# Kernel optimization log

Measured on AMD Instinct MI355X. Metric: run time of the kernel, lower is better.

Reference implementation:

```python
import jax, jax.numpy as jnp
import numpy as np

N = 8192
E = 262144
D_IN = 256
D_OUT = 256

def setup_inputs() -> dict:
    key = jax.random.key(0)
    k1, k2, k3, k4 = jax.random.split(key, 4)
    x = jax.random.normal(k1, (N, D_IN), dtype=jnp.float32)
    edge_index = jax.random.randint(k2, (2, E), 0, N, dtype=jnp.int64)
    W = jax.random.normal(k3, (D_OUT, D_IN), dtype=jnp.float32) * (1.0 / np.sqrt(D_IN))
    b = jax.random.normal(k4, (D_OUT,), dtype=jnp.float32) * 0.01
    return {"x": x, "edge_index": edge_index, "W": W, "b": b}

def reference(x, edge_index, W, b):
    num_nodes = x.shape[0]
    # dense adjacency: adj[src, dst] = 1.0 (duplicates collapse to 1, matching torch assignment)
    adj = jnp.zeros((num_nodes, num_nodes), dtype=x.dtype)
    adj = adj.at[edge_index[0], edge_index[1]].set(1.0)
    adj = adj + jnp.eye(num_nodes, dtype=x.dtype)  # self-loops (may yield 2.0 if edge had self-loop, as in torch)
    deg = adj.sum(axis=1, keepdims=True)           # [N, 1]
    adj_norm = adj / deg                           # row-normalized
    aggregated = adj_norm @ x                      # [N, D_IN]
    return aggregated @ W.T + b                    # linear: [N, D_OUT]
```

## Files before the change

### kernel.cpp

```cpp
#include <hip/hip_runtime.h>
#include <hip/hip_fp16.h>


#define NNODES 8192
#define DFEAT  256
#define WPR    256
#define LISTCAP 2048

typedef __attribute__((ext_vector_type(8))) _Float16 f16x8;
typedef __attribute__((ext_vector_type(4))) _Float16 f16x4;
typedef __attribute__((ext_vector_type(4))) float    f32x4;

__global__ __launch_bounds__(256) void gcn_scatter_wconv(
    const int* __restrict__ ei, int E, unsigned* __restrict__ bitmap,
    const float* __restrict__ W, _Float16* __restrict__ Wh,
    _Float16* __restrict__ Wl) {
  const int nbs = (E + 255) >> 8;
  const int b = blockIdx.x;
  if (b < nbs) {
    int e = b * 256 + threadIdx.x;
    if (e < E) {
      int s = ei[e];
      int d = ei[E + e];
      atomicOr(&bitmap[(size_t)s * WPR + (d >> 5)], 1u << (d & 31));
    }
  } else {
    int i = (b - nbs) * 256 + threadIdx.x;
    if (i < DFEAT * DFEAT / 4) {
      float4 v = *(const float4*)(W + (size_t)i * 4);
      f16x4 h = {(_Float16)v.x, (_Float16)v.y, (_Float16)v.z, (_Float16)v.w};
      f16x4 l = {(_Float16)(v.x - (float)h[0]), (_Float16)(v.y - (float)h[1]),
                 (_Float16)(v.z - (float)h[2]), (_Float16)(v.w - (float)h[3])};
      *(f16x4*)(Wh + (size_t)i * 4) = h;
      *(f16x4*)(Wl + (size_t)i * 4) = l;
    }
  }
}

__global__ __launch_bounds__(256) void gcn_gemm(
    const float* __restrict__ X, const _Float16* __restrict__ Wh,
    const _Float16* __restrict__ Wl, _Float16* __restrict__ Y) {
  const int wave = threadIdx.x >> 6;
  const int lane = threadIdx.x & 63;
  const int row0 = blockIdx.x * 64 + wave * 16;
  const int col0 = blockIdx.y * 64;
  const int lr = lane & 15;
  const int kh = (lane >> 4) * 8;

  f32x4 acc[4];
#pragma unroll
  for (int i = 0; i < 4; ++i) acc[i] = (f32x4){0.f, 0.f, 0.f, 0.f};

  const float*    ap  = X  + (size_t)(row0 + lr) * DFEAT + kh;
  const _Float16* bhp = Wh + (size_t)(col0 + lr) * DFEAT + kh;
  const _Float16* blp = Wl + (size_t)(col0 + lr) * DFEAT + kh;

#pragma unroll
  for (int k0 = 0; k0 < DFEAT; k0 += 32) {
    float4 x0 = *(const float4*)(ap + k0);
    float4 x1 = *(const float4*)(ap + k0 + 4);
    f16x8 a = {(_Float16)x0.x, (_Float16)x0.y, (_Float16)x0.z, (_Float16)x0.w,
               (_Float16)x1.x, (_Float16)x1.y, (_Float16)x1.z, (_Float16)x1.w};
#pragma unroll
    for (int nt = 0; nt < 4; ++nt) {
      f16x8 bh = *(const f16x8*)(bhp + k0 + nt * 16 * DFEAT);
      f16x8 bl = *(const f16x8*)(blp + k0 + nt * 16 * DFEAT);
      acc[nt] = __builtin_amdgcn_mfma_f32_16x16x32_f16(a, bh, acc[nt], 0, 0, 0);
      acc[nt] = __builtin_amdgcn_mfma_f32_16x16x32_f16(a, bl, acc[nt], 0, 0, 0);
    }
  }

  const int crow = row0 + (lane >> 4) * 4;
  const int ccol = col0 + lr;
#pragma unroll
  for (int nt = 0; nt < 4; ++nt)
#pragma unroll
    for (int r = 0; r < 4; ++r)
      Y[(size_t)(crow + r) * DFEAT + ccol + nt * 16] = (_Float16)acc[nt][r];
}

__global__ __launch_bounds__(256) void gcn_aggregate(
    const unsigned* __restrict__ bitmap, const _Float16* __restrict__ Y,
    const float* __restrict__ bias, float* __restrict__ out) {
  __shared__ unsigned short list[LISTCAP];
  __shared__ int cnt;
  const int node = blockIdx.x;
  const int tid  = threadIdx.x;
  if (tid == 0) cnt = 0;
  __syncthreads();

  unsigned w = bitmap[(size_t)node * WPR + tid];
  while (w) {
    int bit = __ffs(w) - 1;
    w &= w - 1;
    int pos = atomicAdd(&cnt, 1);
    if (pos < LISTCAP) list[pos] = (unsigned short)(tid * 32 + bit);
  }
  __syncthreads();

  const int n = min(cnt, LISTCAP);
  float a0 = (float)Y[(size_t)node * DFEAT + tid];
  float a1 = 0.f, a2 = 0.f, a3 = 0.f;
  int k = 0;
  for (; k + 4 <= n; k += 4) {
    int j0 = list[k], j1 = list[k + 1], j2 = list[k + 2], j3 = list[k + 3];
    a0 += (float)Y[(size_t)j0 * DFEAT + tid];
    a1 += (float)Y[(size_t)j1 * DFEAT + tid];
    a2 += (float)Y[(size_t)j2 * DFEAT + tid];
    a3 += (float)Y[(size_t)j3 * DFEAT + tid];
  }
  for (; k < n; ++k) a0 += (float)Y[(size_t)list[k] * DFEAT + tid];

  out[(size_t)node * DFEAT + tid] =
      (a0 + a1 + a2 + a3) / (float)(n + 1) + bias[tid];
}

extern "C" void kernel_launch(void* const* d_in, const int* in_sizes, int n_in,
                              void* d_out, int out_size, void* d_ws, size_t ws_size,
                              hipStream_t stream) {
  const float* x  = (const float*)d_in[0];
  const int*   ei = (const int*)d_in[1];
  const float* W  = (const float*)d_in[2];
  const float* b  = (const float*)d_in[3];
  float* out = (float*)d_out;
  const int E = in_sizes[1] / 2;

  char* p = (char*)d_ws;
  size_t off = 0;
  auto take = [&](size_t bytes) { char* r = p + off; off = (off + bytes + 255) & ~(size_t)255; return r; };
  unsigned* bitmap = (unsigned*) take((size_t)NNODES * WPR * 4);
  _Float16* Wh     = (_Float16*) take((size_t)DFEAT * DFEAT * 2);
  _Float16* Wl     = (_Float16*) take((size_t)DFEAT * DFEAT * 2);
  _Float16* Y      = (_Float16*) take((size_t)NNODES * DFEAT * 2);

  hipMemsetAsync(bitmap, 0, (size_t)NNODES * WPR * 4, stream);

  const int nbs = (E + 255) / 256;
  const int nbw = (DFEAT * DFEAT / 4 + 255) / 256;
  gcn_scatter_wconv<<<nbs + nbw, 256, 0, stream>>>(ei, E, bitmap, W, Wh, Wl);

  gcn_gemm<<<dim3(NNODES / 64, DFEAT / 64), 256, 0, stream>>>(x, Wh, Wl, Y);

  gcn_aggregate<<<NNODES, 256, 0, stream>>>(bitmap, Y, b, out);
}
```

Baseline: 121.6 us.

## Fuse GCN stages into persistent kernel with capped adjacency lists

Replaces the three launches plus bitmap memset with one persistent kernel of 512 blocks. Stages are separated by atomic-counter grid barriers. The dense 8192x8192-bit adjacency bitmap becomes per-node fixed-capacity neighbour lists built with atomic degree counters, and duplicate edges are removed at aggregation time by an in-wave quadratic scan. This drops the large bitmap memset and scan plus the launch gaps. The cost is spin-wait barriers and a degree cap of 192 that silently truncates higher-degree nodes. The control-word reset using a magic value may also race across repeated calls.

```diff
diff --git a/kernel.cpp b/kernel.cpp
--- a/kernel.cpp
+++ b/kernel.cpp
@@ -4,115 +4,164 @@
 
 #define NNODES 8192
 #define DFEAT  256
-#define WPR    256
-#define LISTCAP 2048
+#define MAXDEG 192
+#define NBLK   512
+#define NTHR   256
+#define MAGIC  0x13572468u
 
 typedef __attribute__((ext_vector_type(8))) _Float16 f16x8;
 typedef __attribute__((ext_vector_type(4))) _Float16 f16x4;
 typedef __attribute__((ext_vector_type(4))) float    f32x4;
 
-__global__ __launch_bounds__(256) void gcn_scatter_wconv(
-    const int* __restrict__ ei, int E, unsigned* __restrict__ bitmap,
-    const float* __restrict__ W, _Float16* __restrict__ Wh,
-    _Float16* __restrict__ Wl) {
-  const int nbs = (E + 255) >> 8;
-  const int b = blockIdx.x;
-  if (b < nbs) {
-    int e = b * 256 + threadIdx.x;
-    if (e < E) {
-      int s = ei[e];
-      int d = ei[E + e];
-      atomicOr(&bitmap[(size_t)s * WPR + (d >> 5)], 1u << (d & 31));
+__device__ inline void grid_barrier(unsigned* ctr) {
+  __syncthreads();
+  if (threadIdx.x == 0) {
+    __threadfence();
+    atomicAdd(ctr, 1u);
+    while (atomicAdd(ctr, 0u) < NBLK) __builtin_amdgcn_s_sleep(8);
+    __threadfence();
+  }
+  __syncthreads();
+}
+
+__global__ __launch_bounds__(NTHR, 2) void gcn_all(
+    const float* __restrict__ X, const int* __restrict__ ei,
+    const float* __restrict__ W, const float* __restrict__ bias, int E,
+    unsigned* __restrict__ ctl, int* __restrict__ deg,
+    unsigned short* __restrict__ adj, _Float16* __restrict__ Wh,
+    _Float16* __restrict__ Wl, _Float16* __restrict__ Y,
+    float* __restrict__ out)
+{
+  const int bid  = blockIdx.x, tid = threadIdx.x;
+  const int gtid = bid * NTHR + tid;
+  const int wave = tid >> 6, lane = tid & 63;
+
+  if (gtid < NNODES) deg[gtid] = 0;
+  if (gtid < DFEAT * DFEAT / 4) {
+    float4 v = *(const float4*)(W + (size_t)gtid * 4);
+    f16x4 h = {(_Float16)v.x, (_Float16)v.y, (_Float16)v.z, (_Float16)v.w};
+    f16x4 l = {(_Float16)(v.x - (float)h[0]), (_Float16)(v.y - (float)h[1]),
+               (_Float16)(v.z - (float)h[2]), (_Float16)(v.w - (float)h[3])};
+    *(f16x4*)(Wh + (size_t)gtid * 4) = h;
+    *(f16x4*)(Wl + (size_t)gtid * 4) = l;
+  }
+  if (bid == 0) {
+    __syncthreads();
+    if (tid >= 1 && tid <= 3) ctl[tid * 32] = 0;
+    __syncthreads();
+    if (tid == 0) { __threadfence(); atomicExch(&ctl[0], MAGIC); }
+  }
+  if (tid == 0)
+    while (atomicAdd(&ctl[0], 0u) != MAGIC) __builtin_amdgcn_s_sleep(8);
+  __syncthreads();
+  grid_barrier(&ctl[32]);
+
+  for (int e = gtid; e < E; e += NBLK * NTHR) {
+    int s = ei[e];
+    int d = ei[E + e];
+    int pos = atomicAdd(&deg[s], 1);
+    if (pos < MAXDEG) adj[(size_t)s * MAXDEG + pos] = (unsigned short)d;
+  }
+  grid_barrier(&ctl[64]);
+
+  {
+    const int row0 = (bid >> 2) * 64 + wave * 16;
+    const int col0 = (bid & 3) * 64;
+    const int lr = lane & 15;
+    const int kh = (lane >> 4) * 8;
+
+    f32x4 acc[4];
+#pragma unroll
+    for (int i = 0; i < 4; ++i) acc[i] = (f32x4){0.f, 0.f, 0.f, 0.f};
+
+    const float*    ap  = X  + (size_t)(row0 + lr) * DFEAT + kh;
+    const _Float16* bhp = Wh + (size_t)(col0 + lr) * DFEAT + kh;
+    const _Float16* blp = Wl + (size_t)(col0 + lr) * DFEAT + kh;
+
+#pragma unroll
+    for (int k0 = 0; k0 < DFEAT; k0 += 32) {
+      float4 x0 = *(const float4*)(ap + k0);
+      float4 x1 = *(const float4*)(ap + k0 + 4);
+      f16x8 a = {(_Float16)x0.x, (_Float16)x0.y, (_Float16)x0.z, (_Float16)x0.w,
+                 (_Float16)x1.x, (_Float16)x1.y, (_Float16)x1.z, (_Float16)x1.w};
+#pragma unroll
+      for (int nt = 0; nt < 4; ++nt) {
+        f16x8 bh = *(const f16x8*)(bhp + k0 + nt * 16 * DFEAT);
+        f16x8 bl = *(const f16x8*)(blp + k0 + nt * 16 * DFEAT);
+        acc[nt] = __builtin_amdgcn_mfma_f32_16x16x32_f16(a, bh, acc[nt], 0, 0, 0);
+        acc[nt] = __builtin_amdgcn_mfma_f32_16x16x32_f16(a, bl, acc[nt], 0, 0, 0);
+      }
     }
-  } else {
-    int i = (b - nbs) * 256 + threadIdx.x;
-    if (i < DFEAT * DFEAT / 4) {
-      float4 v = *(const float4*)(W + (size_t)i * 4);
-      f16x4 h = {(_Float16)v.x, (_Float16)v.y, (_Float16)v.z, (_Float16)v.w};
-      f16x4 l = {(_Float16)(v.x - (float)h[0]), (_Float16)(v.y - (float)h[1]),
-                 (_Float16)(v.z - (float)h[2]), (_Float16)(v.w - (float)h[3])};
-      *(f16x4*)(Wh + (size_t)i * 4) = h;
-      *(f16x4*)(Wl + (size_t)i * 4) = l;
+    const int crow = row0 + (lane >> 4) * 4;
+    const int ccol = col0 + lr;
+#pragma unroll
+    for (int nt = 0; nt < 4; ++nt)
+#pragma unroll
+      for (int r = 0; r < 4; ++r)
+        Y[(size_t)(crow + r) * DFEAT + ccol + nt * 16] = (_Float16)acc[nt][r];
+  }
+  grid_barrier(&ctl[96]);
+
+  {
+    __shared__ unsigned short listS[4][MAXDEG];
+    __shared__ unsigned char  keepS[4][MAXDEG];
+    unsigned short* list = listS[wave];
+    unsigned char*  keep = keepS[wave];
+    const int ch4 = lane * 4;
+    const float4 b4 = *(const float4*)(bias + ch4);
+
+    for (int node = bid * 4 + wave; node < NNODES; node += NBLK * 4) {
+      int d = atomicAdd(&deg[node], 0);
+      if (d > MAXDEG) d = MAXDEG;
+
+      for (int base = 0; base < d; base += 64)
+        if (base + lane < d)
+          list[base + lane] = adj[(size_t)node * MAXDEG + base + lane];
+
+      int ndist = 0;
+#pragma unroll
+      for (int base = 0; base < MAXDEG; base += 64) {
+        int idx = base + lane;
+        bool kp = false;
+        if (idx < d) {
+          unsigned short v = list[idx];
+          kp = true;
+          for (int k = 0; k < idx; ++k)
+            if (list[k] == v) { kp = false; break; }
+        }
+        keep[idx] = kp ? 1 : 0;
+        ndist += __popcll(__ballot(kp));
+      }
+
+      f16x4 sv = *(const f16x4*)(Y + (size_t)node * DFEAT + ch4);
+      float ax = (float)sv[0], ay = (float)sv[1], az = (float)sv[2], aw = (float)sv[3];
+
+      int k = 0;
+      for (; k + 4 <= d; k += 4) {
+        int j0 = list[k], j1 = list[k + 1], j2 = list[k + 2], j3 = list[k + 3];
+        float w0 = keep[k], w1 = keep[k + 1], w2 = keep[k + 2], w3 = keep[k + 3];
+        f16x4 r0 = *(const f16x4*)(Y + (size_t)j0 * DFEAT + ch4);
+        f16x4 r1 = *(const f16x4*)(Y + (size_t)j1 * DFEAT + ch4);
+        f16x4 r2 = *(const f16x4*)(Y + (size_t)j2 * DFEAT + ch4);
+        f16x4 r3 = *(const f16x4*)(Y + (size_t)j3 * DFEAT + ch4);
+        ax += w0 * (float)r0[0] + w1 * (float)r1[0] + w2 * (float)r2[0] + w3 * (float)r3[0];
+        ay += w0 * (float)r0[1] + w1 * (float)r1[1] + w2 * (float)r2[1] + w3 * (float)r3[1];
+        az += w0 * (float)r0[2] + w1 * (float)r1[2] + w2 * (float)r2[2] + w3 * (float)r3[2];
+        aw += w0 * (float)r0[3] + w1 * (float)r1[3] + w2 * (float)r2[3] + w3 * (float)r3[3];
+      }
+      for (; k < d; ++k) {
+        float w0 = keep[k];
+        f16x4 r0 = *(const f16x4*)(Y + (size_t)list[k] * DFEAT + ch4);
+        ax += w0 * (float)r0[0]; ay += w0 * (float)r0[1];
+        az += w0 * (float)r0[2]; aw += w0 * (float)r0[3];
+      }
+
+      float inv = 1.f / (float)(ndist + 1);
+      float4 o = {ax * inv + b4.x, ay * inv + b4.y,
+                  az * inv + b4.z, aw * inv + b4.w};
+      *(float4*)(out + (size_t)node * DFEAT + ch4) = o;
     }
   }
-}
-
-__global__ __launch_bounds__(256) void gcn_gemm(
-    const float* __restrict__ X, const _Float16* __restrict__ Wh,
-    const _Float16* __restrict__ Wl, _Float16* __restrict__ Y) {
-  const int wave = threadIdx.x >> 6;
-  const int lane = threadIdx.x & 63;
-  const int row0 = blockIdx.x * 64 + wave * 16;
-  const int col0 = blockIdx.y * 64;
-  const int lr = lane & 15;
-  const int kh = (lane >> 4) * 8;
-
-  f32x4 acc[4];
-#pragma unroll
-  for (int i = 0; i < 4; ++i) acc[i] = (f32x4){0.f, 0.f, 0.f, 0.f};
-
-  const float*    ap  = X  + (size_t)(row0 + lr) * DFEAT + kh;
-  const _Float16* bhp = Wh + (size_t)(col0 + lr) * DFEAT + kh;
-  const _Float16* blp = Wl + (size_t)(col0 + lr) * DFEAT + kh;
-
-#pragma unroll
-  for (int k0 = 0; k0 < DFEAT; k0 += 32) {
-    float4 x0 = *(const float4*)(ap + k0);
-    float4 x1 = *(const float4*)(ap + k0 + 4);
-    f16x8 a = {(_Float16)x0.x, (_Float16)x0.y, (_Float16)x0.z, (_Float16)x0.w,
-               (_Float16)x1.x, (_Float16)x1.y, (_Float16)x1.z, (_Float16)x1.w};
-#pragma unroll
-    for (int nt = 0; nt < 4; ++nt) {
-      f16x8 bh = *(const f16x8*)(bhp + k0 + nt * 16 * DFEAT);
-      f16x8 bl = *(const f16x8*)(blp + k0 + nt * 16 * DFEAT);
-      acc[nt] = __builtin_amdgcn_mfma_f32_16x16x32_f16(a, bh, acc[nt], 0, 0, 0);
-      acc[nt] = __builtin_amdgcn_mfma_f32_16x16x32_f16(a, bl, acc[nt], 0, 0, 0);
-    }
-  }
-
-  const int crow = row0 + (lane >> 4) * 4;
-  const int ccol = col0 + lr;
-#pragma unroll
-  for (int nt = 0; nt < 4; ++nt)
-#pragma unroll
-    for (int r = 0; r < 4; ++r)
-      Y[(size_t)(crow + r) * DFEAT + ccol + nt * 16] = (_Float16)acc[nt][r];
-}
-
-__global__ __launch_bounds__(256) void gcn_aggregate(
-    const unsigned* __restrict__ bitmap, const _Float16* __restrict__ Y,
-    const float* __restrict__ bias, float* __restrict__ out) {
-  __shared__ unsigned short list[LISTCAP];
-  __shared__ int cnt;
-  const int node = blockIdx.x;
-  const int tid  = threadIdx.x;
-  if (tid == 0) cnt = 0;
-  __syncthreads();
-
-  unsigned w = bitmap[(size_t)node * WPR + tid];
-  while (w) {
-    int bit = __ffs(w) - 1;
-    w &= w - 1;
-    int pos = atomicAdd(&cnt, 1);
-    if (pos < LISTCAP) list[pos] = (unsigned short)(tid * 32 + bit);
-  }
-  __syncthreads();
-
-  const int n = min(cnt, LISTCAP);
-  float a0 = (float)Y[(size_t)node * DFEAT + tid];
-  float a1 = 0.f, a2 = 0.f, a3 = 0.f;
-  int k = 0;
-  for (; k + 4 <= n; k += 4) {
-    int j0 = list[k], j1 = list[k + 1], j2 = list[k + 2], j3 = list[k + 3];
-    a0 += (float)Y[(size_t)j0 * DFEAT + tid];
-    a1 += (float)Y[(size_t)j1 * DFEAT + tid];
-    a2 += (float)Y[(size_t)j2 * DFEAT + tid];
-    a3 += (float)Y[(size_t)j3 * DFEAT + tid];
-  }
-  for (; k < n; ++k) a0 += (float)Y[(size_t)list[k] * DFEAT + tid];
-
-  out[(size_t)node * DFEAT + tid] =
-      (a0 + a1 + a2 + a3) / (float)(n + 1) + bias[tid];
 }
 
 extern "C" void kernel_launch(void* const* d_in, const int* in_sizes, int n_in,
@@ -128,18 +177,12 @@
   char* p = (char*)d_ws;
   size_t off = 0;
   auto take = [&](size_t bytes) { char* r = p + off; off = (off + bytes + 255) & ~(size_t)255; return r; };
-  unsigned* bitmap = (unsigned*) take((size_t)NNODES * WPR * 4);
-  _Float16* Wh     = (_Float16*) take((size_t)DFEAT * DFEAT * 2);
-  _Float16* Wl     = (_Float16*) take((size_t)DFEAT * DFEAT * 2);
-  _Float16* Y      = (_Float16*) take((size_t)NNODES * DFEAT * 2);
+  unsigned*       ctl = (unsigned*)       take(512);
+  int*            deg = (int*)            take((size_t)NNODES * 4);
+  unsigned short* adj = (unsigned short*) take((size_t)NNODES * MAXDEG * 2);
+  _Float16*       Wh  = (_Float16*)       take((size_t)DFEAT * DFEAT * 2);
+  _Float16*       Wl  = (_Float16*)       take((size_t)DFEAT * DFEAT * 2);
+  _Float16*       Y   = (_Float16*)       take((size_t)NNODES * DFEAT * 2);
 
-  hipMemsetAsync(bitmap, 0, (size_t)NNODES * WPR * 4, stream);
-
-  const int nbs = (E + 255) / 256;
-  const int nbw = (DFEAT * DFEAT / 4 + 255) / 256;
-  gcn_scatter_wconv<<<nbs + nbw, 256, 0, stream>>>(ei, E, bitmap, W, Wh, Wl);
-
-  gcn_gemm<<<dim3(NNODES / 64, DFEAT / 64), 256, 0, stream>>>(x, Wh, Wl, Y);
-
-  gcn_aggregate<<<NNODES, 256, 0, stream>>>(bitmap, Y, b, out);
+  gcn_all<<<NBLK, NTHR, 0, stream>>>(x, ei, W, b, E, ctl, deg, adj, Wh, Wl, Y, out);
 }
```

New measurement: 262.8 us. 2.16x slower.

## Fuse bitmap zeroing and W conversion into GEMM, wave-per-node aggregation

Applied to the files above, without the earlier changes.

Drops the memset and folds bitmap zeroing into the GEMM kernel. The W fp16 hi/lo split now happens inline in the GEMM, which uses wider 64x128 tiles. Edge scatter becomes its own launch. Aggregation now assigns one wave per node with f16x4 vectorized gathers, and the per-node neighbor list cap drops to 256. This is meant to cut launch count and improve gather efficiency, at the cost of recomputing the W conversion per block and risking truncation for nodes with more than 256 neighbors.

```diff
diff --git a/kernel.cpp b/kernel.cpp
--- a/kernel.cpp
+++ b/kernel.cpp
@@ -5,55 +5,36 @@
 #define NNODES 8192
 #define DFEAT  256
 #define WPR    256
-#define LISTCAP 2048
+#define LISTCAP 256
 
 typedef __attribute__((ext_vector_type(8))) _Float16 f16x8;
 typedef __attribute__((ext_vector_type(4))) _Float16 f16x4;
 typedef __attribute__((ext_vector_type(4))) float    f32x4;
 
-__global__ __launch_bounds__(256) void gcn_scatter_wconv(
-    const int* __restrict__ ei, int E, unsigned* __restrict__ bitmap,
-    const float* __restrict__ W, _Float16* __restrict__ Wh,
-    _Float16* __restrict__ Wl) {
-  const int nbs = (E + 255) >> 8;
-  const int b = blockIdx.x;
-  if (b < nbs) {
-    int e = b * 256 + threadIdx.x;
-    if (e < E) {
-      int s = ei[e];
-      int d = ei[E + e];
-      atomicOr(&bitmap[(size_t)s * WPR + (d >> 5)], 1u << (d & 31));
-    }
-  } else {
-    int i = (b - nbs) * 256 + threadIdx.x;
-    if (i < DFEAT * DFEAT / 4) {
-      float4 v = *(const float4*)(W + (size_t)i * 4);
-      f16x4 h = {(_Float16)v.x, (_Float16)v.y, (_Float16)v.z, (_Float16)v.w};
-      f16x4 l = {(_Float16)(v.x - (float)h[0]), (_Float16)(v.y - (float)h[1]),
-                 (_Float16)(v.z - (float)h[2]), (_Float16)(v.w - (float)h[3])};
-      *(f16x4*)(Wh + (size_t)i * 4) = h;
-      *(f16x4*)(Wl + (size_t)i * 4) = l;
-    }
+__global__ __launch_bounds__(256) void gcn_gemm(
+    const float* __restrict__ X, const float* __restrict__ W,
+    _Float16* __restrict__ Y, uint4* __restrict__ bitmap4) {
+  const int bid = blockIdx.x, tid = threadIdx.x;
+  const int gtid = bid * 256 + tid;
+
+  {
+    const uint4 z = {0u, 0u, 0u, 0u};
+#pragma unroll
+    for (int i = 0; i < 8; ++i) bitmap4[(size_t)gtid * 8 + i] = z;
   }
-}
 
-__global__ __launch_bounds__(256) void gcn_gemm(
-    const float* __restrict__ X, const _Float16* __restrict__ Wh,
-    const _Float16* __restrict__ Wl, _Float16* __restrict__ Y) {
-  const int wave = threadIdx.x >> 6;
-  const int lane = threadIdx.x & 63;
-  const int row0 = blockIdx.x * 64 + wave * 16;
-  const int col0 = blockIdx.y * 64;
+  const int wave = tid >> 6, lane = tid & 63;
+  const int row0 = (bid >> 1) * 64 + wave * 16;
+  const int col0 = (bid & 1) * 128;
   const int lr = lane & 15;
   const int kh = (lane >> 4) * 8;
 
-  f32x4 acc[4];
+  f32x4 acc[8];
 #pragma unroll
-  for (int i = 0; i < 4; ++i) acc[i] = (f32x4){0.f, 0.f, 0.f, 0.f};
+  for (int i = 0; i < 8; ++i) acc[i] = (f32x4){0.f, 0.f, 0.f, 0.f};
 
-  const float*    ap  = X  + (size_t)(row0 + lr) * DFEAT + kh;
-  const _Float16* bhp = Wh + (size_t)(col0 + lr) * DFEAT + kh;
-  const _Float16* blp = Wl + (size_t)(col0 + lr) * DFEAT + kh;
+  const float* ap = X + (size_t)(row0 + lr) * DFEAT + kh;
+  const float* wp = W + (size_t)(col0 + lr) * DFEAT + kh;
 
 #pragma unroll
   for (int k0 = 0; k0 < DFEAT; k0 += 32) {
@@ -62,9 +43,15 @@
     f16x8 a = {(_Float16)x0.x, (_Float16)x0.y, (_Float16)x0.z, (_Float16)x0.w,
                (_Float16)x1.x, (_Float16)x1.y, (_Float16)x1.z, (_Float16)x1.w};
 #pragma unroll
-    for (int nt = 0; nt < 4; ++nt) {
-      f16x8 bh = *(const f16x8*)(bhp + k0 + nt * 16 * DFEAT);
-      f16x8 bl = *(const f16x8*)(blp + k0 + nt * 16 * DFEAT);
+    for (int nt = 0; nt < 8; ++nt) {
+      float4 w0 = *(const float4*)(wp + k0 + nt * 16 * DFEAT);
+      float4 w1 = *(const float4*)(wp + k0 + nt * 16 * DFEAT + 4);
+      f16x8 bh = {(_Float16)w0.x, (_Float16)w0.y, (_Float16)w0.z, (_Float16)w0.w,
+                  (_Float16)w1.x, (_Float16)w1.y, (_Float16)w1.z, (_Float16)w1.w};
+      f16x8 bl = {(_Float16)(w0.x - (float)bh[0]), (_Float16)(w0.y - (float)bh[1]),
+                  (_Float16)(w0.z - (float)bh[2]), (_Float16)(w0.w - (float)bh[3]),
+                  (_Float16)(w1.x - (float)bh[4]), (_Float16)(w1.y - (float)bh[5]),
+                  (_Float16)(w1.z - (float)bh[6]), (_Float16)(w1.w - (float)bh[7])};
       acc[nt] = __builtin_amdgcn_mfma_f32_16x16x32_f16(a, bh, acc[nt], 0, 0, 0);
       acc[nt] = __builtin_amdgcn_mfma_f32_16x16x32_f16(a, bl, acc[nt], 0, 0, 0);
     }
@@ -73,46 +60,83 @@
   const int crow = row0 + (lane >> 4) * 4;
   const int ccol = col0 + lr;
 #pragma unroll
-  for (int nt = 0; nt < 4; ++nt)
+  for (int nt = 0; nt < 8; ++nt)
 #pragma unroll
     for (int r = 0; r < 4; ++r)
       Y[(size_t)(crow + r) * DFEAT + ccol + nt * 16] = (_Float16)acc[nt][r];
 }
 
+__global__ __launch_bounds__(256) void gcn_scatter(
+    const int* __restrict__ ei, int E, unsigned* __restrict__ bitmap) {
+  int e = blockIdx.x * 256 + threadIdx.x;
+  if (e < E) {
+    int s = ei[e];
+    int d = ei[E + e];
+    atomicOr(&bitmap[(size_t)s * WPR + (d >> 5)], 1u << (d & 31));
+  }
+}
+
 __global__ __launch_bounds__(256) void gcn_aggregate(
     const unsigned* __restrict__ bitmap, const _Float16* __restrict__ Y,
     const float* __restrict__ bias, float* __restrict__ out) {
-  __shared__ unsigned short list[LISTCAP];
-  __shared__ int cnt;
-  const int node = blockIdx.x;
-  const int tid  = threadIdx.x;
-  if (tid == 0) cnt = 0;
-  __syncthreads();
+  __shared__ unsigned short listS[4][LISTCAP];
+  __shared__ int cntS[4];
 
-  unsigned w = bitmap[(size_t)node * WPR + tid];
-  while (w) {
-    int bit = __ffs(w) - 1;
-    w &= w - 1;
-    int pos = atomicAdd(&cnt, 1);
-    if (pos < LISTCAP) list[pos] = (unsigned short)(tid * 32 + bit);
+  const int tid = threadIdx.x;
+  const int wave = tid >> 6, lane = tid & 63;
+  const int node = blockIdx.x * 4 + wave;
+  unsigned short* list = listS[wave];
+
+  if (lane == 0) cntS[wave] = 0;
+  uint4 wv = *(const uint4*)(bitmap + (size_t)node * WPR + lane * 4);
+  unsigned ws[4] = {wv.x, wv.y, wv.z, wv.w};
+#pragma unroll
+  for (int q = 0; q < 4; ++q) {
+    unsigned w = ws[q];
+    int base = (lane * 4 + q) * 32;
+    while (w) {
+      int bit = __ffs(w) - 1;
+      w &= w - 1;
+      int pos = atomicAdd(&cntS[wave], 1);
+      if (pos < LISTCAP) list[pos] = (unsigned short)(base + bit);
+    }
   }
   __syncthreads();
 
-  const int n = min(cnt, LISTCAP);
-  float a0 = (float)Y[(size_t)node * DFEAT + tid];
-  float a1 = 0.f, a2 = 0.f, a3 = 0.f;
+  const int n = min(cntS[wave], LISTCAP);
+  const int ch4 = lane * 4;
+
+  f16x4 sv = *(const f16x4*)(Y + (size_t)node * DFEAT + ch4);
+  f32x4 a0 = {(float)sv[0], (float)sv[1], (float)sv[2], (float)sv[3]};
+  f32x4 a1 = {0.f, 0.f, 0.f, 0.f}, a2 = a1, a3 = a1;
+
   int k = 0;
   for (; k + 4 <= n; k += 4) {
     int j0 = list[k], j1 = list[k + 1], j2 = list[k + 2], j3 = list[k + 3];
-    a0 += (float)Y[(size_t)j0 * DFEAT + tid];
-    a1 += (float)Y[(size_t)j1 * DFEAT + tid];
-    a2 += (float)Y[(size_t)j2 * DFEAT + tid];
-    a3 += (float)Y[(size_t)j3 * DFEAT + tid];
+    f16x4 r0 = *(const f16x4*)(Y + (size_t)j0 * DFEAT + ch4);
+    f16x4 r1 = *(const f16x4*)(Y + (size_t)j1 * DFEAT + ch4);
+    f16x4 r2 = *(const f16x4*)(Y + (size_t)j2 * DFEAT + ch4);
+    f16x4 r3 = *(const f16x4*)(Y + (size_t)j3 * DFEAT + ch4);
+#pragma unroll
+    for (int c = 0; c < 4; ++c) {
+      a0[c] += (float)r0[c]; a1[c] += (float)r1[c];
+      a2[c] += (float)r2[c]; a3[c] += (float)r3[c];
+    }
   }
-  for (; k < n; ++k) a0 += (float)Y[(size_t)list[k] * DFEAT + tid];
+  for (; k < n; ++k) {
+    f16x4 r0 = *(const f16x4*)(Y + (size_t)list[k] * DFEAT + ch4);
+#pragma unroll
+    for (int c = 0; c < 4; ++c) a0[c] += (float)r0[c];
+  }
 
-  out[(size_t)node * DFEAT + tid] =
-      (a0 + a1 + a2 + a3) / (float)(n + 1) + bias[tid];
+  const float inv = 1.f / (float)(n + 1);
+  const float4 b4 = *(const float4*)(bias + ch4);
+  float4 o;
+  o.x = (a0[0] + a1[0] + a2[0] + a3[0]) * inv + b4.x;
+  o.y = (a0[1] + a1[1] + a2[1] + a3[1]) * inv + b4.y;
+  o.z = (a0[2] + a1[2] + a2[2] + a3[2]) * inv + b4.z;
+  o.w = (a0[3] + a1[3] + a2[3] + a3[3]) * inv + b4.w;
+  *(float4*)(out + (size_t)node * DFEAT + ch4) = o;
 }
 
 extern "C" void kernel_launch(void* const* d_in, const int* in_sizes, int n_in,
@@ -129,17 +153,9 @@
   size_t off = 0;
   auto take = [&](size_t bytes) { char* r = p + off; off = (off + bytes + 255) & ~(size_t)255; return r; };
   unsigned* bitmap = (unsigned*) take((size_t)NNODES * WPR * 4);
-  _Float16* Wh     = (_Float16*) take((size_t)DFEAT * DFEAT * 2);
-  _Float16* Wl     = (_Float16*) take((size_t)DFEAT * DFEAT * 2);
   _Float16* Y      = (_Float16*) take((size_t)NNODES * DFEAT * 2);
 
-  hipMemsetAsync(bitmap, 0, (size_t)NNODES * WPR * 4, stream);
-
-  const int nbs = (E + 255) / 256;
-  const int nbw = (DFEAT * DFEAT / 4 + 255) / 256;
-  gcn_scatter_wconv<<<nbs + nbw, 256, 0, stream>>>(ei, E, bitmap, W, Wh, Wl);
-
-  gcn_gemm<<<dim3(NNODES / 64, DFEAT / 64), 256, 0, stream>>>(x, Wh, Wl, Y);
-
-  gcn_aggregate<<<NNODES, 256, 0, stream>>>(bitmap, Y, b, out);
+  gcn_gemm<<<256, 256, 0, stream>>>(x, W, Y, (uint4*)bitmap);
+  gcn_scatter<<<(E + 255) / 256, 256, 0, stream>>>(ei, E, bitmap);
+  gcn_aggregate<<<NNODES / 4, 256, 0, stream>>>(bitmap, Y, b, out);
 }
```

Result: faster. 108.6 us (-10.7%).
